# Kernel tuning notes

Measured on AMD Instinct MI355X. Metric: run time of the kernel, lower is better.

## Reference

```python
import jax, jax.numpy as jnp
import numpy as np

BATCH, SEQ, L_IN, M_ENC, H_DIM, F_MLP = 16, 2048, 256, 512, 1024, 4096
LN_EPS = 1e-5


def setup_inputs() -> dict:
    key = jax.random.key(0)
    ks = jax.random.split(key, 13)
    x = jax.random.normal(ks[0], (BATCH, SEQ, L_IN), dtype=jnp.float32)
    W_enc = jax.random.normal(ks[1], (L_IN, M_ENC), dtype=jnp.float32) / np.sqrt(L_IN)
    b_enc = jnp.zeros((M_ENC,), dtype=jnp.float32)
    W_B = jax.random.normal(ks[2], (M_ENC, H_DIM), dtype=jnp.float32) / np.sqrt(M_ENC)
    # fixed reservoir matrix, scaled for spectral radius < 1
    A = jax.random.normal(ks[3], (H_DIM, H_DIM), dtype=jnp.float32) * (0.99 / np.sqrt(H_DIM))
    W_res = jax.random.normal(ks[4], (L_IN, H_DIM), dtype=jnp.float32) / np.sqrt(L_IN)
    b_res = jnp.zeros((H_DIM,), dtype=jnp.float32)
    ln_g = jnp.ones((H_DIM,), dtype=jnp.float32)
    ln_b = jnp.zeros((H_DIM,), dtype=jnp.float32)
    W1 = jax.random.normal(ks[5], (H_DIM, F_MLP), dtype=jnp.float32) / np.sqrt(H_DIM)
    b1 = jnp.zeros((F_MLP,), dtype=jnp.float32)
    W2 = jax.random.normal(ks[6], (F_MLP, H_DIM), dtype=jnp.float32) / np.sqrt(F_MLP)
    b2 = jnp.zeros((H_DIM,), dtype=jnp.float32)
    return {"x": x, "W_enc": W_enc, "b_enc": b_enc, "W_B": W_B, "A": A,
            "W_res": W_res, "b_res": b_res, "ln_g": ln_g, "ln_b": ln_b,
            "W1": W1, "b1": b1, "W2": W2, "b2": b2}


def reference(x, W_enc, b_enc, W_B, A, W_res, b_res, ln_g, ln_b, W1, b1, W2, b2):
    # encoder + B applied to all timesteps at once: [B,S,H]
    Bu = (jnp.einsum('bsl,lm->bsm', x, W_enc) + b_enc) @ W_B
    # linear recurrence h_t = h_{t-1} @ A + Bu_t, h_0 = Bu_0 (zeros init works)
    Bu_t = jnp.swapaxes(Bu, 0, 1)  # [S,B,H]

    def step(h, bu):
        h = h @ A + bu
        return h, h

    h0 = jnp.zeros((x.shape[0], A.shape[0]), dtype=x.dtype)
    _, Hs = jax.lax.scan(step, h0, Bu_t)
    H_seq_pre = jnp.swapaxes(Hs, 0, 1)  # [B,S,H]

    residual = jnp.einsum('bsl,lh->bsh', x, W_res) + b_res
    z = H_seq_pre + residual
    mu = jnp.mean(z, axis=-1, keepdims=True)
    var = jnp.var(z, axis=-1, keepdims=True)
    H_seq = (z - mu) * jax.lax.rsqrt(var + LN_EPS) * ln_g + ln_b

    h_last = H_seq[:, -1, :]
    out = jax.nn.relu(h_last @ W1 + b1) @ W2 + b2
    return out, H_seq_pre
```

## Files before the change

kernel.cpp:

```cpp
#include <hip/hip_runtime.h>
#include <math.h>

#define BATCH 16
#define SEQ   2048
#define L_INP 256
#define MENC  512
#define HD    1024
#define FM    4096
#define TCH   16
#define NCH   128
#define NROW  (BATCH*NCH)

typedef unsigned short u16;
typedef __attribute__((ext_vector_type(8))) short s8v;
typedef __attribute__((ext_vector_type(4))) float f4v;

__device__ inline u16 bf16_rne(float x) {
    unsigned u = __builtin_bit_cast(unsigned, x);
    u += 0x7fff + ((u >> 16) & 1);
    return (u16)(u >> 16);
}
__device__ inline float bf16_tof(u16 h) {
    unsigned u = ((unsigned)h) << 16;
    return __builtin_bit_cast(float, u);
}
__device__ inline void split2(float x, u16& h, u16& l) {
    h = bf16_rne(x);
    l = bf16_rne(x - bf16_tof(h));
}

__device__ inline void gload_lds16(const u16* g, u16* l) {
    __builtin_amdgcn_global_load_lds(
        (const __attribute__((address_space(1))) void*)g,
        (__attribute__((address_space(3))) void*)l, 16, 0, 0);
}

#define TS 64
#define KT 16
#define LP 68
__device__ inline float4 add4(float4 a, float4 b) {
    return make_float4(a.x + b.x, a.y + b.y, a.z + b.z, a.w + b.w);
}
template<int MODE>
__global__ __launch_bounds__(256)
void gemm_k(const float* __restrict__ IN, const float* __restrict__ W,
            float* __restrict__ OUT, const float* __restrict__ BIAS,
            int M, int N, int K, int ldIN)
{
    __shared__ float As[KT][LP];
    __shared__ float Bs[KT][LP];
    const int tid  = threadIdx.x;
    const int tx   = tid & 15, ty = tid >> 4;
    const int col0 = blockIdx.x * TS;
    const int row0 = blockIdx.y * TS;
    const int la_k = tid & 15, la_r = tid >> 4;
    const int lb_j = tid & 63, lb_k = tid >> 6;
    float acc[4][4] = {};

    for (int k0 = 0; k0 < K; k0 += KT) {
        #pragma unroll
        for (int i = 0; i < 4; ++i) {
            int r = la_r + (i << 4);
            int grow = row0 + r;
            float v = 0.f;
            if (grow < M) v = IN[(long)grow * ldIN + k0 + la_k];
            As[la_k][r] = v;
        }
        #pragma unroll
        for (int i = 0; i < 4; ++i) {
            int k = lb_k + (i << 2);
            Bs[k][lb_j] = W[(long)(k0 + k) * N + col0 + lb_j];
        }
        __syncthreads();
        #pragma unroll
        for (int kk = 0; kk < KT; ++kk) {
            float4 av = *(const float4*)&As[kk][ty << 2];
            float4 bv = *(const float4*)&Bs[kk][tx << 2];
            float ar[4] = {av.x, av.y, av.z, av.w};
            float br[4] = {bv.x, bv.y, bv.z, bv.w};
            #pragma unroll
            for (int i = 0; i < 4; ++i)
                #pragma unroll
                for (int j = 0; j < 4; ++j)
                    acc[i][j] = fmaf(ar[i], br[j], acc[i][j]);
        }
        __syncthreads();
    }
    const int jc = col0 + (tx << 2);
    float4 bias4 = make_float4(0.f, 0.f, 0.f, 0.f);
    if constexpr (MODE == 1 || MODE == 2) bias4 = *(const float4*)&BIAS[jc];
    #pragma unroll
    for (int i = 0; i < 4; ++i) {
        int row = row0 + (ty << 2) + i;
        if (row >= M) continue;
        float4 vv = make_float4(acc[i][0], acc[i][1], acc[i][2], acc[i][3]);
        if constexpr (MODE == 1 || MODE == 2) vv = add4(vv, bias4);
        if constexpr (MODE == 2) {
            vv.x = fmaxf(vv.x, 0.f); vv.y = fmaxf(vv.y, 0.f);
            vv.z = fmaxf(vv.z, 0.f); vv.w = fmaxf(vv.w, 0.f);
        }
        *(float4*)&OUT[(long)row * N + jc] = vv;
    }
}

template<int KC>
__global__ __launch_bounds__(256)
void skgemm(const float* __restrict__ IN, const float* __restrict__ W,
            float* __restrict__ PART, int M, int N, int ldIN)
{
    const int tid = threadIdx.x;
    const int m   = tid >> 4;
    const int cq  = tid & 15;
    const int col = blockIdx.x * 64 + cq * 4;
    const int p   = blockIdx.y;
    const int k0  = p * KC;
    __shared__ float sIN[16 * KC];
    #pragma unroll
    for (int i = tid; i < 16 * KC; i += 256) {
        int mm = i / KC, kk = i - mm * KC;
        sIN[i] = (mm < M) ? IN[(long)mm * ldIN + k0 + kk] : 0.f;
    }
    __syncthreads();
    float4 acc = make_float4(0.f, 0.f, 0.f, 0.f);
    const float* wp = W + (long)k0 * N + col;
    #pragma unroll 4
    for (int k = 0; k < KC; ++k) {
        float a = sIN[m * KC + k];
        float4 w4 = *(const float4*)&wp[(long)k * N];
        acc.x = fmaf(a, w4.x, acc.x);
        acc.y = fmaf(a, w4.y, acc.y);
        acc.z = fmaf(a, w4.z, acc.z);
        acc.w = fmaf(a, w4.w, acc.w);
    }
    *(float4*)&PART[((long)p * 16 + m) * N + col] = acc;
}

template<int MODE>
__global__ __launch_bounds__(256)
void skred(const float* __restrict__ PART, const float* __restrict__ BIAS,
           float* __restrict__ OUT, int M, int N, int P)
{
    long i = (long)blockIdx.x * 256 + threadIdx.x;
    if (i >= (long)M * N) return;
    int mm = (int)(i / N), n = (int)(i - (long)mm * N);
    float s = 0.f;
    for (int p = 0; p < P; ++p) s += PART[((long)p * 16 + mm) * N + n];
    if constexpr (MODE == 1 || MODE == 2) s += BIAS[n];
    if constexpr (MODE == 2) s = fmaxf(s, 0.f);
    OUT[(long)mm * N + n] = s;
}

#define LK 32
template<int MODE, int KDIM>
__global__ __launch_bounds__(256)
void pgemm(const u16* __restrict__ INh, const u16* __restrict__ INl,
           const u16* __restrict__ Wh,  const u16* __restrict__ Wl,
           float* __restrict__ HOUT,
           const u16* __restrict__ EXh, const u16* __restrict__ EXl,
           u16* __restrict__ Oh, u16* __restrict__ Ol,
           u16* __restrict__ OTh, u16* __restrict__ OTl,
           const float* __restrict__ BIAS,
           int t, int dshift, int inslot, int oslot)
{
    const int tid = threadIdx.x;
    const int z = blockIdx.z;
    if constexpr (MODE == 0) {
        long oin = ((long)(inslot + z)) << 20;
        INh += oin; INl += oin;
        long oo = ((long)(oslot + z)) << 20;
        Oh += oo; Ol += oo; OTh += oo; OTl += oo;
    }
    if constexpr (MODE == 3) {
        long ow = ((long)z) << 20;
        Wh += ow; Wl += ow;
    }
    const int row0 = blockIdx.y * 64;
    const int col0 = blockIdx.x * 64;

    __shared__ u16 sAh[64 * LK], sAl[64 * LK], sBh[64 * LK], sBl[64 * LK];

    const int lane = tid & 63;
    const int wv   = tid >> 6;
    const int wrow = (wv >> 1) << 5;
    const int wcol = (wv & 1) << 5;
    const int fl   = lane & 15;
    const int quad = lane >> 4;

    const int srow = lane >> 2;
    const int sq   = lane & 3;
    const int qsw  = sq ^ ((lane >> 3) & 3);
    const int rin  = wv * 16 + srow;
    int gA = row0 + rin;
    if constexpr (MODE == 2 || MODE == 3) { gA -= dshift; if (gA < 0) gA = 0; }
    const long offA = (long)gA * KDIM + qsw * 8;
    const long offB = (long)(col0 + rin) * KDIM + qsw * 8;
    const int  lb   = (wv * 16) * LK;

    const int fsw = (quad ^ ((fl >> 1) & 3)) << 3;

    bool dead[2] = {false, false};
    if constexpr (MODE == 2 || MODE == 3) {
        #pragma unroll
        for (int mt = 0; mt < 2; ++mt)
            dead[mt] = (row0 + wrow + mt * 16 + fl) < dshift;
    }

    f4v acc[2][2] = {};
    const s8v zer = {0, 0, 0, 0, 0, 0, 0, 0};

    for (int k0 = 0; k0 < KDIM; k0 += 32) {
        __syncthreads();
        gload_lds16(INh + offA + k0, &sAh[lb]);
        gload_lds16(INl + offA + k0, &sAl[lb]);
        gload_lds16(Wh  + offB + k0, &sBh[lb]);
        gload_lds16(Wl  + offB + k0, &sBl[lb]);
        __syncthreads();
        s8v ah[2], al[2], bh[2], bl[2];
        #pragma unroll
        for (int mt = 0; mt < 2; ++mt) {
            int off = (wrow + mt * 16 + fl) * LK + fsw;
            ah[mt] = *(const s8v*)&sAh[off];
            al[mt] = *(const s8v*)&sAl[off];
            if constexpr (MODE == 2 || MODE == 3) {
                if (dead[mt]) { ah[mt] = zer; al[mt] = zer; }
            }
        }
        #pragma unroll
        for (int nt = 0; nt < 2; ++nt) {
            int off = (wcol + nt * 16 + fl) * LK + fsw;
            bh[nt] = *(const s8v*)&sBh[off];
            bl[nt] = *(const s8v*)&sBl[off];
        }
        #pragma unroll
        for (int mt = 0; mt < 2; ++mt)
            #pragma unroll
            for (int nt = 0; nt < 2; ++nt) {
                acc[mt][nt] = __builtin_amdgcn_mfma_f32_16x16x32_bf16(ah[mt], bh[nt], acc[mt][nt], 0, 0, 0);
                acc[mt][nt] = __builtin_amdgcn_mfma_f32_16x16x32_bf16(ah[mt], bl[nt], acc[mt][nt], 0, 0, 0);
                acc[mt][nt] = __builtin_amdgcn_mfma_f32_16x16x32_bf16(al[mt], bh[nt], acc[mt][nt], 0, 0, 0);
            }
    }

    #pragma unroll
    for (int mt = 0; mt < 2; ++mt) {
        #pragma unroll
        for (int nt = 0; nt < 2; ++nt) {
            #pragma unroll
            for (int reg = 0; reg < 4; ++reg) {
                int grow = row0 + wrow + mt * 16 + quad * 4 + reg;
                int gcol = col0 + wcol + nt * 16 + fl;
                float v = acc[mt][nt][reg];
                if constexpr (MODE == 0) {
                    u16 h, l; split2(v, h, l);
                    long o  = ((long)grow << 10) + gcol;
                    long ot = ((long)gcol << 10) + grow;
                    Oh[o] = h; Ol[o] = l;
                    OTh[ot] = h; OTl[ot] = l;
                } else if constexpr (MODE == 1) {
                    int b = grow & 15, c = grow >> 4;
                    long exoff = ((long)(b * SEQ + c * TCH + t) << 10) + gcol;
                    v += HOUT[exoff];
                    HOUT[exoff] = v;
                    long o = ((long)grow << 10) + gcol;
                    u16 h, l; split2(v, h, l);
                    Oh[o] = h; Ol[o] = l;
                } else if constexpr (MODE == 2) {
                    long o = ((long)grow << 10) + gcol;
                    v += bf16_tof(EXh[o]) + bf16_tof(EXl[o]);
                    u16 h, l; split2(v, h, l);
                    Oh[o] = h; Ol[o] = l;
                } else if constexpr (MODE == 3) {
                    if (grow >= 16) {
                        int b = grow & 15, c = grow >> 4;
                        long exoff = ((long)(b * SEQ + c * TCH + z) << 10) + gcol;
                        HOUT[exoff] += v;
                    }
                } else {
                    v += BIAS[gcol];
                    HOUT[((long)grow << 10) + gcol] = v;
                    if ((grow & 15) == 0) {
                        int b = grow >> 11;
                        int s = grow & (SEQ - 1);
                        long so = ((long)(s + b) << 10) + gcol;
                        u16 h, l; split2(v, h, l);
                        Oh[so] = h; Ol[so] = l;
                    }
                }
            }
        }
    }
}

__global__ __launch_bounds__(256)
void splitA_k(const float* __restrict__ A, u16* __restrict__ nH, u16* __restrict__ nL,
              u16* __restrict__ tH, u16* __restrict__ tL)
{
    __shared__ unsigned sm[64][65];
    const int r0 = blockIdx.y * 64, c0 = blockIdx.x * 64;
    const int tr = threadIdx.x >> 4;
    const int tc = (threadIdx.x & 15) * 4;
    #pragma unroll
    for (int i = 0; i < 4; ++i) {
        int row = tr + i * 16;
        float4 v = *(const float4*)&A[((long)(r0 + row) << 10) + c0 + tc];
        float vv[4] = {v.x, v.y, v.z, v.w};
        u16 h[4], l[4];
        #pragma unroll
        for (int j = 0; j < 4; ++j) {
            split2(vv[j], h[j], l[j]);
            sm[row][tc + j] = (((unsigned)h[j]) << 16) | l[j];
        }
        long o = ((long)(r0 + row) << 10) + c0 + tc;
        *(uint2*)&nH[o] = make_uint2((unsigned)h[0] | ((unsigned)h[1] << 16),
                                     (unsigned)h[2] | ((unsigned)h[3] << 16));
        *(uint2*)&nL[o] = make_uint2((unsigned)l[0] | ((unsigned)l[1] << 16),
                                     (unsigned)l[2] | ((unsigned)l[3] << 16));
    }
    __syncthreads();
    #pragma unroll
    for (int i = 0; i < 4; ++i) {
        int n = tr + i * 16;
        unsigned p[4];
        #pragma unroll
        for (int j = 0; j < 4; ++j) p[j] = sm[tc + j][n];
        long o = ((long)(c0 + n) << 10) + r0 + tc;
        *(uint2*)&tH[o] = make_uint2((p[0] >> 16) | (p[1] & 0xffff0000u),
                                     (p[2] >> 16) | (p[3] & 0xffff0000u));
        *(uint2*)&tL[o] = make_uint2((p[0] & 0xffffu) | (p[1] << 16),
                                     (p[2] & 0xffffu) | (p[3] << 16));
    }
}

__global__ __launch_bounds__(256)
void splitX_k(const float* __restrict__ X, u16* __restrict__ xh, u16* __restrict__ xl)
{
    long i4 = (long)blockIdx.x * 256 + threadIdx.x;
    long base = i4 * 4;
    float4 v = *(const float4*)&X[base];
    float vv[4] = {v.x, v.y, v.z, v.w};
    u16 h[4], l[4];
    #pragma unroll
    for (int j = 0; j < 4; ++j) split2(vv[j], h[j], l[j]);
    *(uint2*)&xh[base] = make_uint2((unsigned)h[0] | ((unsigned)h[1] << 16),
                                    (unsigned)h[2] | ((unsigned)h[3] << 16));
    *(uint2*)&xl[base] = make_uint2((unsigned)l[0] | ((unsigned)l[1] << 16),
                                    (unsigned)l[2] | ((unsigned)l[3] << 16));
}

__global__ __launch_bounds__(256)
void splitWt_k(const float* __restrict__ Wf, u16* __restrict__ th, u16* __restrict__ tl)
{
    int i = blockIdx.x * 256 + threadIdx.x;
    int n = i >> 8, k = i & 255;
    float v = Wf[((long)k << 10) + n];
    u16 h, l; split2(v, h, l);
    th[i] = h; tl[i] = l;
}

__global__ __launch_bounds__(256)
void ln_k(const u16* __restrict__ Sh, const u16* __restrict__ Sl,
          const float* __restrict__ Rlast,
          const float* __restrict__ g, const float* __restrict__ bta,
          float* __restrict__ zout)
{
    __shared__ double red[256];
    int b = blockIdx.x, tid = threadIdx.x;
    long base = ((long)((NCH - 1) * BATCH + b)) << 10;
    const float* rr = Rlast + b * HD;
    double s = 0.0;
    for (int j = tid; j < HD; j += 256)
        s += (double)(bf16_tof(Sh[base + j]) + bf16_tof(Sl[base + j])) + (double)rr[j];
    red[tid] = s; __syncthreads();
    for (int o = 128; o > 0; o >>= 1) { if (tid < o) red[tid] += red[tid + o]; __syncthreads(); }
    double mu = red[0] * (1.0 / HD);
    __syncthreads();
    double ss = 0.0;
    for (int j = tid; j < HD; j += 256) {
        double zz = (double)(bf16_tof(Sh[base + j]) + bf16_tof(Sl[base + j])) + (double)rr[j] - mu;
        ss += zz * zz;
    }
    red[tid] = ss; __syncthreads();
    for (int o = 128; o > 0; o >>= 1) { if (tid < o) red[tid] += red[tid + o]; __syncthreads(); }
    double inv = 1.0 / sqrt(red[0] * (1.0 / HD) + 1e-5);
    __syncthreads();
    for (int j = tid; j < HD; j += 256) {
        double zz = (double)(bf16_tof(Sh[base + j]) + bf16_tof(Sl[base + j])) + (double)rr[j];
        zout[b * HD + j] = (float)(((zz - mu) * inv) * (double)g[j] + (double)bta[j]);
    }
}

extern "C" void kernel_launch(void* const* d_in, const int* in_sizes, int n_in,
                              void* d_out, int out_size, void* d_ws, size_t ws_size,
                              hipStream_t stream)
{
    const float* x     = (const float*)d_in[0];
    const float* W_enc = (const float*)d_in[1];
    const float* b_enc = (const float*)d_in[2];
    const float* W_B   = (const float*)d_in[3];
    const float* A     = (const float*)d_in[4];
    const float* W_res = (const float*)d_in[5];
    const float* b_res = (const float*)d_in[6];
    const float* ln_g  = (const float*)d_in[7];
    const float* ln_b  = (const float*)d_in[8];
    const float* W1    = (const float*)d_in[9];
    const float* b1    = (const float*)d_in[10];
    const float* W2    = (const float*)d_in[11];
    const float* b2    = (const float*)d_in[12];

    float* out0 = (float*)d_out;
    float* Hout = out0 + (long)BATCH * HD;

    char* p = (char*)d_ws;
    auto alloc = [&](size_t bytes) { void* r = (void*)p; p += (bytes + 255) & ~(size_t)255; return r; };
    const long M2 = 1L << 20;
    u16* natH = (u16*)alloc(22 * M2 * 2);
    u16* natL = (u16*)alloc(22 * M2 * 2);
    u16* trH  = (u16*)alloc(22 * M2 * 2);
    u16* trL  = (u16*)alloc(22 * M2 * 2);
    const long SB = (long)NROW * HD;
    u16* SPh[3]; u16* SPl[3];
    for (int i = 0; i < 3; ++i) { SPh[i] = (u16*)alloc(SB * 2); SPl[i] = (u16*)alloc(SB * 2); }
    float* Wf    = (float*)alloc((long)L_INP * HD * 4);
    float* bf    = (float*)alloc(HD * 4);
    float* Rlast = (float*)alloc(BATCH * HD * 4);
    float* zln   = (float*)alloc(BATCH * HD * 4);
    float* t1    = (float*)alloc((long)BATCH * FM * 4);
    float* PART  = (float*)alloc(32L * 16 * 4096 * 4);

    const long MS = (long)BATCH * SEQ;
    u16* xh  = natH;
    u16* xl  = natH + MS * L_INP;
    u16* wth = trH;
    u16* wtl = trH + (long)HD * L_INP;

    dim3 blk(256);

    gemm_k<0><<<dim3(HD / TS, L_INP / TS), blk, 0, stream>>>(W_enc, W_B, Wf, nullptr, L_INP, HD, MENC, MENC);
    skgemm<128><<<dim3(HD / 64, MENC / 128), blk, 0, stream>>>(b_enc, W_B, PART, 1, HD, MENC);
    skred<0><<<dim3((HD + 255) / 256), blk, 0, stream>>>(PART, nullptr, bf, 1, HD, MENC / 128);
    splitWt_k<<<dim3((HD * L_INP) / 256), blk, 0, stream>>>(Wf, wth, wtl);
    splitX_k<<<dim3((int)(MS * L_INP / 4 / 256)), blk, 0, stream>>>(x, xh, xl);
    pgemm<4, L_INP><<<dim3(HD / 64, (int)(MS / 64)), blk, 0, stream>>>(
        xh, xl, wth, wtl, Hout, nullptr, nullptr,
        SPh[0], SPl[0], nullptr, nullptr, bf, 0, 0, 0, 0);

    splitA_k<<<dim3(16, 16), blk, 0, stream>>>(A, natH, natL, trH, trL);

    pgemm<0, HD><<<dim3(16, 16, 1), blk, 0, stream>>>(natH, natL, trH, trL, nullptr, nullptr, nullptr,
                                                      natH, natL, trH, trL, nullptr, 0, 0, 0, 1);
    pgemm<0, HD><<<dim3(16, 16, 2), blk, 0, stream>>>(natH, natL, trH + (1L << 20), trL + (1L << 20), nullptr, nullptr, nullptr,
                                                      natH, natL, trH, trL, nullptr, 0, 0, 0, 2);
    pgemm<0, HD><<<dim3(16, 16, 4), blk, 0, stream>>>(natH, natL, trH + (3L << 20), trL + (3L << 20), nullptr, nullptr, nullptr,
                                                      natH, natL, trH, trL, nullptr, 0, 0, 0, 4);
    pgemm<0, HD><<<dim3(16, 16, 8), blk, 0, stream>>>(natH, natL, trH + (7L << 20), trL + (7L << 20), nullptr, nullptr, nullptr,
                                                      natH, natL, trH, trL, nullptr, 0, 0, 0, 8);
    for (int i = 0; i < 6; ++i) {
        int src = 15 + i;
        pgemm<0, HD><<<dim3(16, 16, 1), blk, 0, stream>>>(natH, natL, trH + ((long)src << 20), trL + ((long)src << 20),
                                                          nullptr, nullptr, nullptr,
                                                          natH, natL, trH, trL, nullptr, 0, 0, src, src + 1);
    }

    int cur = 0, nxt = 1;
    for (int t = 1; t < TCH; ++t) {
        pgemm<1, HD><<<dim3(16, 32), blk, 0, stream>>>(SPh[cur], SPl[cur], trH, trL, Hout, nullptr, nullptr,
                                                       SPh[nxt], SPl[nxt], nullptr, nullptr, nullptr, t, 0, 0, 0);
        int tmp = cur; cur = nxt; nxt = tmp;
    }

    int pin = cur;
    int tgt[2] = { nxt, 2 };
    for (int i = 0; i < 7; ++i) {
        int d = (1 << i) * BATCH;
        int wslot = (i == 0) ? 15 : (16 + i - 1);
        int ob = tgt[i & 1];
        pgemm<2, HD><<<dim3(16, 32), blk, 0, stream>>>(SPh[pin], SPl[pin],
                                                       trH + ((long)wslot << 20), trL + ((long)wslot << 20),
                                                       nullptr, SPh[pin], SPl[pin],
                                                       SPh[ob], SPl[ob], nullptr, nullptr, nullptr, 0, d, 0, 0);
        pin = ob;
    }
    int Sfin = pin;

    pgemm<3, HD><<<dim3(16, 32, TCH), blk, 0, stream>>>(SPh[Sfin], SPl[Sfin], trH, trL, Hout, nullptr, nullptr,
                                                        nullptr, nullptr, nullptr, nullptr, nullptr, 0, BATCH, 0, 0);

    skgemm<64><<<dim3(HD / 64, L_INP / 64), blk, 0, stream>>>(x + (long)(SEQ - 1) * L_INP, W_res, PART, BATCH, HD, SEQ * L_INP);
    skred<1><<<dim3((BATCH * HD + 255) / 256), blk, 0, stream>>>(PART, b_res, Rlast, BATCH, HD, L_INP / 64);
    ln_k<<<dim3(BATCH), blk, 0, stream>>>(SPh[Sfin], SPl[Sfin], Rlast, ln_g, ln_b, zln);
    skgemm<128><<<dim3(FM / 64, HD / 128), blk, 0, stream>>>(zln, W1, PART, BATCH, FM, HD);
    skred<2><<<dim3((BATCH * FM + 255) / 256), blk, 0, stream>>>(PART, b1, t1, BATCH, FM, HD / 128);
    skgemm<128><<<dim3(HD / 64, FM / 128), blk, 0, stream>>>(t1, W2, PART, BATCH, HD, FM);
    skred<1><<<dim3((BATCH * HD + 255) / 256), blk, 0, stream>>>(PART, b2, out0, BATCH, HD, FM / 128);
}
```

Before: 1.601 ms.

## Double-buffer LDS in split-bf16 GEMM and add 128-wide tile variant

Adds an LDS double buffer to the pgemm kernel so the global-to-LDS loads for the next K step overlap with the MFMA work on the current one, and drops one of the two barriers per iteration. Also templates the tile size so the large-grid launches (input projection, the power-of-A products with z=4/8, and the final chunk propagation) use 128x128 tiles for more data reuse. This doubles LDS use per block (and quadruples it for 128 tiles) and raises register pressure from the 4x4 accumulator set, which may lower occupancy.

```diff
diff --git a/kernel.cpp b/kernel.cpp
--- a/kernel.cpp
+++ b/kernel.cpp
@@ -151,7 +151,7 @@
 }
 
 #define LK 32
-template<int MODE, int KDIM>
+template<int MODE, int KDIM, int BT>
 __global__ __launch_bounds__(256)
 void pgemm(const u16* __restrict__ INh, const u16* __restrict__ INl,
            const u16* __restrict__ Wh,  const u16* __restrict__ Wl,
@@ -162,6 +162,9 @@
            const float* __restrict__ BIAS,
            int t, int dshift, int inslot, int oslot)
 {
+    constexpr int MT  = BT / 32;
+    constexpr int NG  = BT / 64;
+    constexpr int BUF = BT * LK;
     const int tid = threadIdx.x;
     const int z = blockIdx.z;
     if constexpr (MODE == 0) {
@@ -174,51 +177,72 @@
         long ow = ((long)z) << 20;
         Wh += ow; Wl += ow;
     }
-    const int row0 = blockIdx.y * 64;
-    const int col0 = blockIdx.x * 64;
-
-    __shared__ u16 sAh[64 * LK], sAl[64 * LK], sBh[64 * LK], sBl[64 * LK];
+    const int row0 = blockIdx.y * BT;
+    const int col0 = blockIdx.x * BT;
+
+    __shared__ u16 sAh[2 * BUF], sAl[2 * BUF], sBh[2 * BUF], sBl[2 * BUF];
 
     const int lane = tid & 63;
     const int wv   = tid >> 6;
-    const int wrow = (wv >> 1) << 5;
-    const int wcol = (wv & 1) << 5;
+    const int wrow = (wv >> 1) * (BT / 2);
+    const int wcol = (wv & 1) * (BT / 2);
     const int fl   = lane & 15;
     const int quad = lane >> 4;
 
     const int srow = lane >> 2;
     const int sq   = lane & 3;
     const int qsw  = sq ^ ((lane >> 3) & 3);
-    const int rin  = wv * 16 + srow;
-    int gA = row0 + rin;
-    if constexpr (MODE == 2 || MODE == 3) { gA -= dshift; if (gA < 0) gA = 0; }
-    const long offA = (long)gA * KDIM + qsw * 8;
-    const long offB = (long)(col0 + rin) * KDIM + qsw * 8;
-    const int  lb   = (wv * 16) * LK;
+    long offA[NG], offB[NG];
+    int  lbs[NG];
+    #pragma unroll
+    for (int h = 0; h < NG; ++h) {
+        int rin = h * 64 + wv * 16 + srow;
+        int gA = row0 + rin;
+        if constexpr (MODE == 2 || MODE == 3) { gA -= dshift; if (gA < 0) gA = 0; }
+        offA[h] = (long)gA * KDIM + qsw * 8;
+        offB[h] = (long)(col0 + rin) * KDIM + qsw * 8;
+        lbs[h]  = (h * 64 + wv * 16) * LK;
+    }
 
     const int fsw = (quad ^ ((fl >> 1) & 3)) << 3;
 
-    bool dead[2] = {false, false};
+    bool dead[MT] = {};
     if constexpr (MODE == 2 || MODE == 3) {
         #pragma unroll
-        for (int mt = 0; mt < 2; ++mt)
+        for (int mt = 0; mt < MT; ++mt)
             dead[mt] = (row0 + wrow + mt * 16 + fl) < dshift;
     }
 
-    f4v acc[2][2] = {};
+    f4v acc[MT][MT] = {};
     const s8v zer = {0, 0, 0, 0, 0, 0, 0, 0};
 
+    #pragma unroll
+    for (int h = 0; h < NG; ++h) {
+        gload_lds16(INh + offA[h], &sAh[lbs[h]]);
+        gload_lds16(INl + offA[h], &sAl[lbs[h]]);
+        gload_lds16(Wh  + offB[h], &sBh[lbs[h]]);
+        gload_lds16(Wl  + offB[h], &sBl[lbs[h]]);
+    }
+    asm volatile("s_waitcnt vmcnt(0)" ::: "memory");
+    __builtin_amdgcn_s_barrier();
+
+    int cur = 0;
     for (int k0 = 0; k0 < KDIM; k0 += 32) {
-        __syncthreads();
-        gload_lds16(INh + offA + k0, &sAh[lb]);
-        gload_lds16(INl + offA + k0, &sAl[lb]);
-        gload_lds16(Wh  + offB + k0, &sBh[lb]);
-        gload_lds16(Wl  + offB + k0, &sBl[lb]);
-        __syncthreads();
-        s8v ah[2], al[2], bh[2], bl[2];
-        #pragma unroll
-        for (int mt = 0; mt < 2; ++mt) {
-            int off = (wrow + mt * 16 + fl) * LK + fsw;
+        const int cb = cur * BUF;
+        const int nb = (cur ^ 1) * BUF;
+        if (k0 + 32 < KDIM) {
+            #pragma unroll
+            for (int h = 0; h < NG; ++h) {
+                gload_lds16(INh + offA[h] + k0 + 32, &sAh[nb + lbs[h]]);
+                gload_lds16(INl + offA[h] + k0 + 32, &sAl[nb + lbs[h]]);
+                gload_lds16(Wh  + offB[h] + k0 + 32, &sBh[nb + lbs[h]]);
+                gload_lds16(Wl  + offB[h] + k0 + 32, &sBl[nb + lbs[h]]);
+            }
+        }
+        s8v ah[MT], al[MT], bh[MT], bl[MT];
+        #pragma unroll
+        for (int mt = 0; mt < MT; ++mt) {
+            int off = cb + (wrow + mt * 16 + fl) * LK + fsw;
             ah[mt] = *(const s8v*)&sAh[off];
             al[mt] = *(const s8v*)&sAl[off];
             if constexpr (MODE == 2 || MODE == 3) {
@@ -226,25 +250,30 @@
             }
         }
         #pragma unroll
-        for (int nt = 0; nt < 2; ++nt) {
-            int off = (wcol + nt * 16 + fl) * LK + fsw;
+        for (int nt = 0; nt < MT; ++nt) {
+            int off = cb + (wcol + nt * 16 + fl) * LK + fsw;
             bh[nt] = *(const s8v*)&sBh[off];
             bl[nt] = *(const s8v*)&sBl[off];
         }
-        #pragma unroll
-        for (int mt = 0; mt < 2; ++mt)
+        asm volatile("s_waitcnt lgkmcnt(0)" ::: "memory");
+        __builtin_amdgcn_sched_barrier(0);
+        #pragma unroll
+        for (int mt = 0; mt < MT; ++mt)
             #pragma unroll
-            for (int nt = 0; nt < 2; ++nt) {
+            for (int nt = 0; nt < MT; ++nt) {
                 acc[mt][nt] = __builtin_amdgcn_mfma_f32_16x16x32_bf16(ah[mt], bh[nt], acc[mt][nt], 0, 0, 0);
                 acc[mt][nt] = __builtin_amdgcn_mfma_f32_16x16x32_bf16(ah[mt], bl[nt], acc[mt][nt], 0, 0, 0);
                 acc[mt][nt] = __builtin_amdgcn_mfma_f32_16x16x32_bf16(al[mt], bh[nt], acc[mt][nt], 0, 0, 0);
             }
-    }
-
-    #pragma unroll
-    for (int mt = 0; mt < 2; ++mt) {
-        #pragma unroll
-        for (int nt = 0; nt < 2; ++nt) {
+        asm volatile("s_waitcnt vmcnt(0)" ::: "memory");
+        __builtin_amdgcn_s_barrier();
+        cur ^= 1;
+    }
+
+    #pragma unroll
+    for (int mt = 0; mt < MT; ++mt) {
+        #pragma unroll
+        for (int nt = 0; nt < MT; ++nt) {
             #pragma unroll
             for (int reg = 0; reg < 4; ++reg) {
                 int grow = row0 + wrow + mt * 16 + quad * 4 + reg;
@@ -440,31 +469,31 @@
     skred<0><<<dim3((HD + 255) / 256), blk, 0, stream>>>(PART, nullptr, bf, 1, HD, MENC / 128);
     splitWt_k<<<dim3((HD * L_INP) / 256), blk, 0, stream>>>(Wf, wth, wtl);
     splitX_k<<<dim3((int)(MS * L_INP / 4 / 256)), blk, 0, stream>>>(x, xh, xl);
-    pgemm<4, L_INP><<<dim3(HD / 64, (int)(MS / 64)), blk, 0, stream>>>(
+    pgemm<4, L_INP, 128><<<dim3(HD / 128, (int)(MS / 128)), blk, 0, stream>>>(
         xh, xl, wth, wtl, Hout, nullptr, nullptr,
         SPh[0], SPl[0], nullptr, nullptr, bf, 0, 0, 0, 0);
 
     splitA_k<<<dim3(16, 16), blk, 0, stream>>>(A, natH, natL, trH, trL);
 
-    pgemm<0, HD><<<dim3(16, 16, 1), blk, 0, stream>>>(natH, natL, trH, trL, nullptr, nullptr, nullptr,
-                                                      natH, natL, trH, trL, nullptr, 0, 0, 0, 1);
-    pgemm<0, HD><<<dim3(16, 16, 2), blk, 0, stream>>>(natH, natL, trH + (1L << 20), trL + (1L << 20), nullptr, nullptr, nullptr,
-                                                      natH, natL, trH, trL, nullptr, 0, 0, 0, 2);
-    pgemm<0, HD><<<dim3(16, 16, 4), blk, 0, stream>>>(natH, natL, trH + (3L << 20), trL + (3L << 20), nullptr, nullptr, nullptr,
-                                                      natH, natL, trH, trL, nullptr, 0, 0, 0, 4);
-    pgemm<0, HD><<<dim3(16, 16, 8), blk, 0, stream>>>(natH, natL, trH + (7L << 20), trL + (7L << 20), nullptr, nullptr, nullptr,
-                                                      natH, natL, trH, trL, nullptr, 0, 0, 0, 8);
+    pgemm<0, HD, 64><<<dim3(16, 16, 1), blk, 0, stream>>>(natH, natL, trH, trL, nullptr, nullptr, nullptr,
+                                                          natH, natL, trH, trL, nullptr, 0, 0, 0, 1);
+    pgemm<0, HD, 64><<<dim3(16, 16, 2), blk, 0, stream>>>(natH, natL, trH + (1L << 20), trL + (1L << 20), nullptr, nullptr, nullptr,
+                                                          natH, natL, trH, trL, nullptr, 0, 0, 0, 2);
+    pgemm<0, HD, 128><<<dim3(8, 8, 4), blk, 0, stream>>>(natH, natL, trH + (3L << 20), trL + (3L << 20), nullptr, nullptr, nullptr,
+                                                         natH, natL, trH, trL, nullptr, 0, 0, 0, 4);
+    pgemm<0, HD, 128><<<dim3(8, 8, 8), blk, 0, stream>>>(natH, natL, trH + (7L << 20), trL + (7L << 20), nullptr, nullptr, nullptr,
+                                                         natH, natL, trH, trL, nullptr, 0, 0, 0, 8);
     for (int i = 0; i < 6; ++i) {
         int src = 15 + i;
-        pgemm<0, HD><<<dim3(16, 16, 1), blk, 0, stream>>>(natH, natL, trH + ((long)src << 20), trL + ((long)src << 20),
-                                                          nullptr, nullptr, nullptr,
-                                                          natH, natL, trH, trL, nullptr, 0, 0, src, src + 1);
+        pgemm<0, HD, 64><<<dim3(16, 16, 1), blk, 0, stream>>>(natH, natL, trH + ((long)src << 20), trL + ((long)src << 20),
+                                                              nullptr, nullptr, nullptr,
+                                                              natH, natL, trH, trL, nullptr, 0, 0, src, src + 1);
     }
 
     int cur = 0, nxt = 1;
     for (int t = 1; t < TCH; ++t) {
-        pgemm<1, HD><<<dim3(16, 32), blk, 0, stream>>>(SPh[cur], SPl[cur], trH, trL, Hout, nullptr, nullptr,
-                                                       SPh[nxt], SPl[nxt], nullptr, nullptr, nullptr, t, 0, 0, 0);
+        pgemm<1, HD, 64><<<dim3(16, 32), blk, 0, stream>>>(SPh[cur], SPl[cur], trH, trL, Hout, nullptr, nullptr,
+                                                           SPh[nxt], SPl[nxt], nullptr, nullptr, nullptr, t, 0, 0, 0);
         int tmp = cur; cur = nxt; nxt = tmp;
     }
 
@@ -474,16 +503,16 @@
         int d = (1 << i) * BATCH;
         int wslot = (i == 0) ? 15 : (16 + i - 1);
         int ob = tgt[i & 1];
-        pgemm<2, HD><<<dim3(16, 32), blk, 0, stream>>>(SPh[pin], SPl[pin],
-                                                       trH + ((long)wslot << 20), trL + ((long)wslot << 20),
-                                                       nullptr, SPh[pin], SPl[pin],
-                                                       SPh[ob], SPl[ob], nullptr, nullptr, nullptr, 0, d, 0, 0);
+        pgemm<2, HD, 64><<<dim3(16, 32), blk, 0, stream>>>(SPh[pin], SPl[pin],
+                                                           trH + ((long)wslot << 20), trL + ((long)wslot << 20),
+                                                           nullptr, SPh[pin], SPl[pin],
+                                                           SPh[ob], SPl[ob], nullptr, nullptr, nullptr, 0, d, 0, 0);
         pin = ob;
     }
     int Sfin = pin;
 
-    pgemm<3, HD><<<dim3(16, 32, TCH), blk, 0, stream>>>(SPh[Sfin], SPl[Sfin], trH, trL, Hout, nullptr, nullptr,
-                                                        nullptr, nullptr, nullptr, nullptr, nullptr, 0, BATCH, 0, 0);
+    pgemm<3, HD, 128><<<dim3(8, 16, TCH), blk, 0, stream>>>(SPh[Sfin], SPl[Sfin], trH, trL, Hout, nullptr, nullptr,
+                                                            nullptr, nullptr, nullptr, nullptr, nullptr, 0, BATCH, 0, 0);
 
     skgemm<64><<<dim3(HD / 64, L_INP / 64), blk, 0, stream>>>(x + (long)(SEQ - 1) * L_INP, W_res, PART, BATCH, HD, SEQ * L_INP);
     skred<1><<<dim3((BATCH * HD + 255) / 256), blk, 0, stream>>>(PART, b_res, Rlast, BATCH, HD, L_INP / 64);
```

Result: no change. 1.581 ms (-1.3%).
